# Kernel tuning notes

Hardware: AMD Instinct MI355X
Metric: run time of the kernel (lower is better)

Reference implementation:

```python
import jax, jax.numpy as jnp
import numpy as np

EMB = 1024
N_HEAD = 16
D_QK = 128  # emb_dim // h_qk
D_V = 128   # emb_dim // h_v


def setup_inputs() -> dict:
    key = jax.random.key(0)
    ks = jax.random.split(key, 9)
    s_in = 1.0 / np.sqrt(EMB)
    s_pr = 1.0 / np.sqrt(N_HEAD * D_V)
    return {
        "X": jax.random.normal(ks[0], (2, 2048, EMB), dtype=jnp.float32),
        "Wq": jax.random.uniform(ks[1], (EMB, N_HEAD * D_QK), jnp.float32, -s_in, s_in),
        "bq": jax.random.uniform(ks[2], (N_HEAD * D_QK,), jnp.float32, -s_in, s_in),
        "Wk": jax.random.uniform(ks[3], (EMB, N_HEAD * D_QK), jnp.float32, -s_in, s_in),
        "bk": jax.random.uniform(ks[4], (N_HEAD * D_QK,), jnp.float32, -s_in, s_in),
        "Wv": jax.random.uniform(ks[5], (EMB, N_HEAD * D_V), jnp.float32, -s_in, s_in),
        "bv": jax.random.uniform(ks[6], (N_HEAD * D_V,), jnp.float32, -s_in, s_in),
        "Wp": jax.random.uniform(ks[7], (N_HEAD * D_V, EMB), jnp.float32, -s_pr, s_pr),
        "bp": jax.random.uniform(ks[8], (EMB,), jnp.float32, -s_pr, s_pr),
    }


def reference(X, Wq, bq, Wk, bk, Wv, bv, Wp, bp):
    b, t, d = X.shape
    # projections -> (b, h, t, dh)
    Q = (X @ Wq + bq).reshape(b, t, N_HEAD, D_QK).transpose(0, 2, 1, 3)
    K = (X @ Wk + bk).reshape(b, t, N_HEAD, D_QK).transpose(0, 2, 1, 3)
    V = (X @ Wv + bv).reshape(b, t, N_HEAD, D_V).transpose(0, 2, 1, 3)
    scale = 1.0 / jnp.sqrt(jnp.asarray(D_QK, X.dtype))
    att = jnp.einsum("bhqd,bhkd->bhqk", Q, K) * scale  # (b,h,t,t)
    causal = jnp.tril(jnp.ones((t, t), dtype=bool))
    att = jnp.where(causal[None, None], att, jnp.asarray(-jnp.inf, att.dtype))
    att = jax.nn.softmax(att, axis=-1)
    y = jnp.einsum("bhqk,bhkd->bhqd", att, V)
    y = y.transpose(0, 2, 1, 3).reshape(b, t, N_HEAD * D_V)
    return y @ Wp + bp
```

## Files before the change

kernel.cpp:

```cpp
#include <hip/hip_runtime.h>
#include <hip/hip_bf16.h>
#include <math.h>

#define EMB   1024
#define NHEAD 16
#define DHEAD 128
#define TSEQ  2048
#define NB    2
#define MROWS (NB * TSEQ)
#define QKVN  (NHEAD * DHEAD)

typedef __bf16 bf16x8 __attribute__((ext_vector_type(8)));
typedef __bf16 bf16x4 __attribute__((ext_vector_type(4)));
typedef float  f32x4  __attribute__((ext_vector_type(4)));

__device__ __forceinline__ unsigned pk_bf16(float a, float b) {
  union { __bf16 h; unsigned short u; } ca, cb;
  ca.h = (__bf16)a; cb.h = (__bf16)b;
  return (unsigned)ca.u | ((unsigned)cb.u << 16);
}

__global__ __launch_bounds__(256) void prep(
    const float* __restrict__ X,
    const float* __restrict__ Wq, const float* __restrict__ Wk,
    const float* __restrict__ Wv, const float* __restrict__ Wp,
    __bf16* __restrict__ Xb, __bf16* __restrict__ Wqt, __bf16* __restrict__ Wkt,
    __bf16* __restrict__ Wvt, __bf16* __restrict__ Wpt) {
  const int z = blockIdx.z;
  if (z == 4) {
    size_t id = ((size_t)(blockIdx.y * 64 + blockIdx.x)) * 2048 + threadIdx.x * 8;
    float4 v0 = *(const float4*)(X + id);
    float4 v1 = *(const float4*)(X + id + 4);
    bf16x8 o = {(__bf16)v0.x, (__bf16)v0.y, (__bf16)v0.z, (__bf16)v0.w,
                (__bf16)v1.x, (__bf16)v1.y, (__bf16)v1.z, (__bf16)v1.w};
    *(bf16x8*)(Xb + id) = o;
    return;
  }
  __shared__ __bf16 tile[32][33];
  const float* in; __bf16* out; int K_, N_, k0, n0;
  if (z < 3) {
    in = z == 0 ? Wq : z == 1 ? Wk : Wv;
    out = z == 0 ? Wqt : z == 1 ? Wkt : Wvt;
    K_ = EMB; N_ = QKVN; k0 = blockIdx.y * 32; n0 = blockIdx.x * 32;
  } else {
    in = Wp; out = Wpt; K_ = QKVN; N_ = EMB; k0 = blockIdx.x * 32; n0 = blockIdx.y * 32;
  }
  const int c = threadIdx.x & 31, r = threadIdx.x >> 5;
#pragma unroll
  for (int i = 0; i < 4; ++i) {
    int kk = r + i * 8;
    tile[kk][c] = (__bf16)in[(size_t)(k0 + kk) * N_ + n0 + c];
  }
  __syncthreads();
#pragma unroll
  for (int i = 0; i < 4; ++i) {
    int nn = r + i * 8;
    out[(size_t)(n0 + nn) * K_ + k0 + c] = tile[c][nn];
  }
}

__device__ __forceinline__ void store1(float* p, float v) { *p = v; }
__device__ __forceinline__ void store1(__bf16* p, float v) { *p = (__bf16)v; }

template <int TM, typename OT, bool VT>
__device__ __forceinline__ void gemm_core(
    const __bf16* __restrict__ A, const __bf16* __restrict__ Bt,
    const float* __restrict__ bias, OT* __restrict__ C,
    int N, int K, int brow, int bcol, float osc,
    __bf16* As, __bf16* Bs) {
  const int tid = threadIdx.x;
  const int wv = tid >> 6, ln = tid & 63;
  const int cl = ln & 15, gp = ln >> 4;
  constexpr int SJ = (TM == 128) ? 4 : 2;
  const int rbase = (TM == 128) ? (wv >> 1) * 64 : 0;
  const int cbase = (TM == 128) ? (wv & 1) * 64 : wv * 32;

  f32x4 acc[4][SJ];
#pragma unroll
  for (int i = 0; i < 4; ++i)
#pragma unroll
    for (int j = 0; j < SJ; ++j) acc[i][j] = (f32x4){0.f, 0.f, 0.f, 0.f};

  for (int k0 = 0; k0 < K; k0 += 64) {
#pragma unroll
    for (int i = 0; i < TM / 32; ++i) {
      int idx = i * 256 + tid;
      int r = idx >> 3, cp = idx & 7, c = cp ^ (r & 7);
      __builtin_amdgcn_global_load_lds(
          (const __attribute__((address_space(1))) unsigned int*)(A + (size_t)(brow + r) * K + k0 + c * 8),
          (__attribute__((address_space(3))) unsigned int*)(As + (size_t)(i * 256 + wv * 64) * 8),
          16, 0, 0);
    }
#pragma unroll
    for (int i = 0; i < 4; ++i) {
      int idx = i * 256 + tid;
      int r = idx >> 3, cp = idx & 7, c = cp ^ (r & 7);
      __builtin_amdgcn_global_load_lds(
          (const __attribute__((address_space(1))) unsigned int*)(Bt + (size_t)(bcol + r) * K + k0 + c * 8),
          (__attribute__((address_space(3))) unsigned int*)(Bs + (size_t)(i * 256 + wv * 64) * 8),
          16, 0, 0);
    }
    __syncthreads();

#pragma unroll
    for (int kc = 0; kc < 2; ++kc) {
      bf16x8 af[4], bfr[SJ];
#pragma unroll
      for (int i = 0; i < 4; ++i) {
        int r = rbase + i * 16 + cl;
        int c = kc * 4 + gp;
        af[i] = *(const bf16x8*)(As + ((size_t)(r * 8 + (c ^ (r & 7)))) * 8);
      }
#pragma unroll
      for (int j = 0; j < SJ; ++j) {
        int r = cbase + j * 16 + cl;
        int c = kc * 4 + gp;
        bfr[j] = *(const bf16x8*)(Bs + ((size_t)(r * 8 + (c ^ (r & 7)))) * 8);
      }
#pragma unroll
      for (int i = 0; i < 4; ++i)
#pragma unroll
        for (int j = 0; j < SJ; ++j)
          acc[i][j] = __builtin_amdgcn_mfma_f32_16x16x32_bf16(af[i], bfr[j], acc[i][j], 0, 0, 0);
    }
    __syncthreads();
  }

  if constexpr (VT) {
#pragma unroll
    for (int j = 0; j < SJ; ++j) {
      int col = bcol + cbase + j * 16 + cl;
      float bb = bias[col];
      int hh = col >> 7, dh = col & 127;
#pragma unroll
      for (int i = 0; i < 4; ++i) {
        int row = brow + rbase + i * 16 + gp * 4;
        int bi = row >> 11, t = row & 2047;
        __bf16* p = (__bf16*)C + ((size_t)((bi * NHEAD + hh) * DHEAD + dh)) * TSEQ + t;
        bf16x4 st = {(__bf16)((acc[i][j][0] + bb) * osc), (__bf16)((acc[i][j][1] + bb) * osc),
                     (__bf16)((acc[i][j][2] + bb) * osc), (__bf16)((acc[i][j][3] + bb) * osc)};
        *(bf16x4*)p = st;
      }
    }
  } else {
#pragma unroll
    for (int j = 0; j < SJ; ++j) {
      int col = bcol + cbase + j * 16 + cl;
      float bb = bias[col];
#pragma unroll
      for (int i = 0; i < 4; ++i) {
#pragma unroll
        for (int rr = 0; rr < 4; ++rr) {
          int row = brow + rbase + i * 16 + gp * 4 + rr;
          store1(C + (size_t)row * N + col, (acc[i][j][rr] + bb) * osc);
        }
      }
    }
  }
}

__global__ __launch_bounds__(256) void gemm_qkv(
    const __bf16* __restrict__ A,
    const __bf16* __restrict__ Wqt, const __bf16* __restrict__ Wkt, const __bf16* __restrict__ Wvt,
    const float* __restrict__ bq, const float* __restrict__ bk, const float* __restrict__ bv,
    __bf16* __restrict__ Q, __bf16* __restrict__ Ko, __bf16* __restrict__ Vt) {
  __shared__ __bf16 As[8192], Bs[8192];
  const int z = blockIdx.z;
  if (z == 0) {
    gemm_core<128, __bf16, false>(A, Wqt, bq, Q, QKVN, EMB, blockIdx.y * 128, blockIdx.x * 128,
                                  0.08838834764831845f, As, Bs);
  } else if (z == 1) {
    gemm_core<128, __bf16, false>(A, Wkt, bk, Ko, QKVN, EMB, blockIdx.y * 128, blockIdx.x * 128,
                                  1.0f, As, Bs);
  } else {
    gemm_core<128, __bf16, true>(A, Wvt, bv, Vt, QKVN, EMB, blockIdx.y * 128, blockIdx.x * 128,
                                 1.0f, As, Bs);
  }
}

__global__ __launch_bounds__(256) void gemm_proj(
    const __bf16* __restrict__ A, const __bf16* __restrict__ Bt,
    const float* __restrict__ bias, float* __restrict__ C) {
  __shared__ __bf16 As[4096], Bs[8192];
  gemm_core<64, float, false>(A, Bt, bias, C, EMB, QKVN, blockIdx.y * 64, blockIdx.x * 128,
                              1.0f, As, Bs);
}

__device__ __forceinline__ void attn_stage(
    const __bf16* __restrict__ Kg, const __bf16* __restrict__ Vg,
    __bf16* Kbuf, __bf16* Vbuf, int kt, int wv, int ln) {
#pragma unroll
  for (int i = 0; i < 4; ++i) {
    int seg = wv * 4 + i;
    int u = seg * 4 + (ln >> 4);
    int slot = ln & 15;
    int xk = slot ^ (u & 15);
    __builtin_amdgcn_global_load_lds(
        (const __attribute__((address_space(1))) unsigned int*)(Kg + (size_t)(kt * 64 + u) * QKVN + xk * 8),
        (__attribute__((address_space(3))) unsigned int*)(Kbuf + seg * 512), 16, 0, 0);
    int d = 2 * u + (xk & 1), c2 = xk >> 1;
    __builtin_amdgcn_global_load_lds(
        (const __attribute__((address_space(1))) unsigned int*)(Vg + (size_t)d * TSEQ + kt * 64 + c2 * 8),
        (__attribute__((address_space(3))) unsigned int*)(Vbuf + seg * 512), 16, 0, 0);
  }
}

__global__ __launch_bounds__(256, 2) void attn_mfma(
    const __bf16* __restrict__ Qb, const __bf16* __restrict__ Kb,
    const __bf16* __restrict__ Vt, __bf16* __restrict__ Y) {
  __shared__ __bf16 Ks[2][8192];
  __shared__ __bf16 Vs[2][8192];

  const int tid = threadIdx.x;
  const int wv = tid >> 6, ln = tid & 63;
  const int cl = ln & 15, gp = ln >> 4;

  const int x = blockIdx.x;
  const int bh = x & 31;
  const int qt = 15 - (x >> 5);
  const int b = bh >> 4, h = bh & 15;
  const int ntiles = 2 * qt + 2;
  const int qloc = qt * 128 + wv * 32;
  const size_t grow = (size_t)b * TSEQ + qloc;

  bf16x8 qa[2][4];
#pragma unroll
  for (int i = 0; i < 2; ++i)
#pragma unroll
    for (int kc = 0; kc < 4; ++kc)
      qa[i][kc] = *(const bf16x8*)(Qb + (grow + i * 16 + cl) * QKVN + h * DHEAD + kc * 32 + gp * 8);

  f32x4 o[2][8];
#pragma unroll
  for (int i = 0; i < 2; ++i)
#pragma unroll
    for (int n = 0; n < 8; ++n) o[i][n] = (f32x4){0.f, 0.f, 0.f, 0.f};
  float l[2] = {0.f, 0.f};

  const __bf16* Kg = Kb + (size_t)b * TSEQ * QKVN + h * DHEAD;
  const __bf16* Vg = Vt + (size_t)bh * DHEAD * TSEQ;

  attn_stage(Kg, Vg, Ks[0], Vs[0], 0, wv, ln);
  __syncthreads();

  const int m0 = 32 * (gp & 1) + cl;
  const int m1 = m0 + 16;
  const bool hi = gp >= 2;

  for (int kt = 0; kt < ntiles; ++kt) {
    const int cur = kt & 1;
    if (kt + 1 < ntiles)
      attn_stage(Kg, Vg, Ks[cur ^ 1], Vs[cur ^ 1], kt + 1, wv, ln);

    if (kt * 64 <= qloc + 31) {
      f32x4 sacc[2][4];
#pragma unroll
      for (int i = 0; i < 2; ++i)
#pragma unroll
        for (int s = 0; s < 4; ++s) sacc[i][s] = (f32x4){0.f, 0.f, 0.f, 0.f};
#pragma unroll
      for (int kc = 0; kc < 4; ++kc) {
#pragma unroll
        for (int s = 0; s < 4; ++s) {
          int r = s * 16 + cl;
          bf16x8 kfr = *(const bf16x8*)(&Ks[cur][r * 128 + (((kc * 4 + gp) ^ (r & 15)) * 8)]);
          sacc[0][s] = __builtin_amdgcn_mfma_f32_16x16x32_bf16(kfr, qa[0][kc], sacc[0][s], 0, 0, 0);
          sacc[1][s] = __builtin_amdgcn_mfma_f32_16x16x32_bf16(kfr, qa[1][kc], sacc[1][s], 0, 0, 0);
        }
      }
      const bool diag = (kt * 64 + 63 > qloc);
      unsigned pk[2][4][2];
#pragma unroll
      for (int i = 0; i < 2; ++i) {
        float psum = 0.f;
        int q = qloc + i * 16 + cl;
#pragma unroll
        for (int s = 0; s < 4; ++s) {
          float e[4];
#pragma unroll
          for (int rg = 0; rg < 4; ++rg) {
            e[rg] = __expf(sacc[i][s][rg]);
            if (diag && (kt * 64 + s * 16 + gp * 4 + rg) > q) e[rg] = 0.f;
            psum += e[rg];
          }
          pk[i][s][0] = pk_bf16(e[0], e[1]);
          pk[i][s][1] = pk_bf16(e[2], e[3]);
        }
        psum += __shfl_xor(psum, 16, 64);
        psum += __shfl_xor(psum, 32, 64);
        l[i] += psum;
      }
#pragma unroll
      for (int k2 = 0; k2 < 2; ++k2) {
        union PU { unsigned u[4]; bf16x8 v; } pf[2];
#pragma unroll
        for (int i = 0; i < 2; ++i) {
          unsigned a0 = __shfl(pk[i][2 * k2][0], m0, 64);
          unsigned b0 = __shfl(pk[i][2 * k2 + 1][0], m0, 64);
          unsigned a1 = __shfl(pk[i][2 * k2][1], m0, 64);
          unsigned b1 = __shfl(pk[i][2 * k2 + 1][1], m0, 64);
          unsigned a2 = __shfl(pk[i][2 * k2][0], m1, 64);
          unsigned b2 = __shfl(pk[i][2 * k2 + 1][0], m1, 64);
          unsigned a3 = __shfl(pk[i][2 * k2][1], m1, 64);
          unsigned b3 = __shfl(pk[i][2 * k2 + 1][1], m1, 64);
          pf[i].u[0] = hi ? b0 : a0;
          pf[i].u[1] = hi ? b1 : a1;
          pf[i].u[2] = hi ? b2 : a2;
          pf[i].u[3] = hi ? b3 : a3;
        }
#pragma unroll
        for (int ds = 0; ds < 8; ++ds) {
          int d = ds * 16 + cl;
          int u = d >> 1;
          int xv = ((k2 * 4 + gp) << 1) | (d & 1);
          bf16x8 vfr = *(const bf16x8*)(&Vs[cur][u * 128 + ((xv ^ (u & 15)) * 8)]);
          o[0][ds] = __builtin_amdgcn_mfma_f32_16x16x32_bf16(vfr, pf[0].v, o[0][ds], 0, 0, 0);
          o[1][ds] = __builtin_amdgcn_mfma_f32_16x16x32_bf16(vfr, pf[1].v, o[1][ds], 0, 0, 0);
        }
      }
    }
    __syncthreads();
  }

#pragma unroll
  for (int i = 0; i < 2; ++i) {
    float inv = 1.0f / l[i];
    __bf16* yrow = Y + (grow + i * 16 + cl) * QKVN + h * DHEAD;
#pragma unroll
    for (int ds = 0; ds < 8; ++ds) {
      bf16x4 st = {(__bf16)(o[i][ds][0] * inv), (__bf16)(o[i][ds][1] * inv),
                   (__bf16)(o[i][ds][2] * inv), (__bf16)(o[i][ds][3] * inv)};
      *(bf16x4*)(yrow + ds * 16 + gp * 4) = st;
    }
  }
}

extern "C" void kernel_launch(void* const* d_in, const int* in_sizes, int n_in,
                              void* d_out, int out_size, void* d_ws, size_t ws_size,
                              hipStream_t stream) {
  const float* X  = (const float*)d_in[0];
  const float* Wq = (const float*)d_in[1];
  const float* bq = (const float*)d_in[2];
  const float* Wk = (const float*)d_in[3];
  const float* bk = (const float*)d_in[4];
  const float* Wv = (const float*)d_in[5];
  const float* bv = (const float*)d_in[6];
  const float* Wp = (const float*)d_in[7];
  const float* bp = (const float*)d_in[8];
  float* out = (float*)d_out;

  const size_t xsz = (size_t)MROWS * EMB;
  const size_t wsz = (size_t)EMB * QKVN;
  const size_t msz = (size_t)MROWS * QKVN;
  __bf16* Xb  = (__bf16*)d_ws;
  __bf16* Wqt = Xb + xsz;
  __bf16* Wkt = Wqt + wsz;
  __bf16* Wvt = Wkt + wsz;
  __bf16* Wpt = Wvt + wsz;
  __bf16* Qb  = Wpt + wsz;
  __bf16* Kb  = Qb + msz;
  __bf16* Vtb = Kb + msz;
  __bf16* Yb  = Vtb + msz;

  dim3 blk(256);

  prep<<<dim3(64, 32, 5), blk, 0, stream>>>(X, Wq, Wk, Wv, Wp, Xb, Wqt, Wkt, Wvt, Wpt);

  gemm_qkv<<<dim3(QKVN / 128, MROWS / 128, 3), blk, 0, stream>>>(
      Xb, Wqt, Wkt, Wvt, bq, bk, bv, Qb, Kb, Vtb);

  attn_mfma<<<dim3(512), blk, 0, stream>>>(Qb, Kb, Vtb, Yb);

  gemm_proj<<<dim3(EMB / 128, MROWS / 64), blk, 0, stream>>>(Yb, Wpt, bp, out);
}
```

Before: 284.9 us.

## Halve attention block to 64 query rows with single-buffered V staging

The attention kernel now runs 2-wave blocks covering 64 query rows, launched as 1024 blocks instead of 512 4-wave blocks of 128 rows. The per-wave skip of fully masked tiles is dropped. V shared memory drops to one buffer, reloaded after an extra barrier once the PV MFMAs finish, while K stays double-buffered. The goal is finer causal load balance and lower LDS use for more resident blocks. The cost is that the V load is no longer overlapped with compute, each iteration has an extra barrier, and K/V tiles are fetched by twice as many blocks.

```diff
diff --git a/kernel.cpp b/kernel.cpp
--- a/kernel.cpp
+++ b/kernel.cpp
@@ -186,18 +186,28 @@
                               1.0f, As, Bs);
 }
 
-__device__ __forceinline__ void attn_stage(
-    const __bf16* __restrict__ Kg, const __bf16* __restrict__ Vg,
-    __bf16* Kbuf, __bf16* Vbuf, int kt, int wv, int ln) {
-#pragma unroll
-  for (int i = 0; i < 4; ++i) {
-    int seg = wv * 4 + i;
+__device__ __forceinline__ void stage_K(
+    const __bf16* __restrict__ Kg, __bf16* Kbuf, int kt, int wv, int ln) {
+#pragma unroll
+  for (int i = 0; i < 8; ++i) {
+    int seg = wv * 8 + i;
     int u = seg * 4 + (ln >> 4);
     int slot = ln & 15;
     int xk = slot ^ (u & 15);
     __builtin_amdgcn_global_load_lds(
         (const __attribute__((address_space(1))) unsigned int*)(Kg + (size_t)(kt * 64 + u) * QKVN + xk * 8),
         (__attribute__((address_space(3))) unsigned int*)(Kbuf + seg * 512), 16, 0, 0);
+  }
+}
+
+__device__ __forceinline__ void stage_V(
+    const __bf16* __restrict__ Vg, __bf16* Vbuf, int kt, int wv, int ln) {
+#pragma unroll
+  for (int i = 0; i < 8; ++i) {
+    int seg = wv * 8 + i;
+    int u = seg * 4 + (ln >> 4);
+    int slot = ln & 15;
+    int xk = slot ^ (u & 15);
     int d = 2 * u + (xk & 1), c2 = xk >> 1;
     __builtin_amdgcn_global_load_lds(
         (const __attribute__((address_space(1))) unsigned int*)(Vg + (size_t)d * TSEQ + kt * 64 + c2 * 8),
@@ -205,11 +215,11 @@
   }
 }
 
-__global__ __launch_bounds__(256, 2) void attn_mfma(
+__global__ __launch_bounds__(128) void attn_mfma(
     const __bf16* __restrict__ Qb, const __bf16* __restrict__ Kb,
     const __bf16* __restrict__ Vt, __bf16* __restrict__ Y) {
   __shared__ __bf16 Ks[2][8192];
-  __shared__ __bf16 Vs[2][8192];
+  __shared__ __bf16 Vs[8192];
 
   const int tid = threadIdx.x;
   const int wv = tid >> 6, ln = tid & 63;
@@ -217,10 +227,10 @@
 
   const int x = blockIdx.x;
   const int bh = x & 31;
-  const int qt = 15 - (x >> 5);
+  const int qt = 31 - (x >> 5);
   const int b = bh >> 4, h = bh & 15;
-  const int ntiles = 2 * qt + 2;
-  const int qloc = qt * 128 + wv * 32;
+  const int ntiles = qt + 1;
+  const int qloc = qt * 64 + wv * 32;
   const size_t grow = (size_t)b * TSEQ + qloc;
 
   bf16x8 qa[2][4];
@@ -240,7 +250,8 @@
   const __bf16* Kg = Kb + (size_t)b * TSEQ * QKVN + h * DHEAD;
   const __bf16* Vg = Vt + (size_t)bh * DHEAD * TSEQ;
 
-  attn_stage(Kg, Vg, Ks[0], Vs[0], 0, wv, ln);
+  stage_K(Kg, Ks[0], 0, wv, ln);
+  stage_V(Vg, Vs, 0, wv, ln);
   __syncthreads();
 
   const int m0 = 32 * (gp & 1) + cl;
@@ -250,75 +261,76 @@
   for (int kt = 0; kt < ntiles; ++kt) {
     const int cur = kt & 1;
     if (kt + 1 < ntiles)
-      attn_stage(Kg, Vg, Ks[cur ^ 1], Vs[cur ^ 1], kt + 1, wv, ln);
-
-    if (kt * 64 <= qloc + 31) {
-      f32x4 sacc[2][4];
-#pragma unroll
-      for (int i = 0; i < 2; ++i)
-#pragma unroll
-        for (int s = 0; s < 4; ++s) sacc[i][s] = (f32x4){0.f, 0.f, 0.f, 0.f};
-#pragma unroll
-      for (int kc = 0; kc < 4; ++kc) {
-#pragma unroll
-        for (int s = 0; s < 4; ++s) {
-          int r = s * 16 + cl;
-          bf16x8 kfr = *(const bf16x8*)(&Ks[cur][r * 128 + (((kc * 4 + gp) ^ (r & 15)) * 8)]);
-          sacc[0][s] = __builtin_amdgcn_mfma_f32_16x16x32_bf16(kfr, qa[0][kc], sacc[0][s], 0, 0, 0);
-          sacc[1][s] = __builtin_amdgcn_mfma_f32_16x16x32_bf16(kfr, qa[1][kc], sacc[1][s], 0, 0, 0);
+      stage_K(Kg, Ks[cur ^ 1], kt + 1, wv, ln);
+
+    f32x4 sacc[2][4];
+#pragma unroll
+    for (int i = 0; i < 2; ++i)
+#pragma unroll
+      for (int s = 0; s < 4; ++s) sacc[i][s] = (f32x4){0.f, 0.f, 0.f, 0.f};
+#pragma unroll
+    for (int kc = 0; kc < 4; ++kc) {
+#pragma unroll
+      for (int s = 0; s < 4; ++s) {
+        int r = s * 16 + cl;
+        bf16x8 kfr = *(const bf16x8*)(&Ks[cur][r * 128 + (((kc * 4 + gp) ^ (r & 15)) * 8)]);
+        sacc[0][s] = __builtin_amdgcn_mfma_f32_16x16x32_bf16(kfr, qa[0][kc], sacc[0][s], 0, 0, 0);
+        sacc[1][s] = __builtin_amdgcn_mfma_f32_16x16x32_bf16(kfr, qa[1][kc], sacc[1][s], 0, 0, 0);
+      }
+    }
+    const bool diag = (kt * 64 + 63 > qloc);
+    unsigned pk[2][4][2];
+#pragma unroll
+    for (int i = 0; i < 2; ++i) {
+      float psum = 0.f;
+      int q = qloc + i * 16 + cl;
+#pragma unroll
+      for (int s = 0; s < 4; ++s) {
+        float e[4];
+#pragma unroll
+        for (int rg = 0; rg < 4; ++rg) {
+          e[rg] = __expf(sacc[i][s][rg]);
+          if (diag && (kt * 64 + s * 16 + gp * 4 + rg) > q) e[rg] = 0.f;
+          psum += e[rg];
         }
-      }
-      const bool diag = (kt * 64 + 63 > qloc);
-      unsigned pk[2][4][2];
+        pk[i][s][0] = pk_bf16(e[0], e[1]);
+        pk[i][s][1] = pk_bf16(e[2], e[3]);
+      }
+      psum += __shfl_xor(psum, 16, 64);
+      psum += __shfl_xor(psum, 32, 64);
+      l[i] += psum;
+    }
+#pragma unroll
+    for (int k2 = 0; k2 < 2; ++k2) {
+      union PU { unsigned u[4]; bf16x8 v; } pf[2];
 #pragma unroll
       for (int i = 0; i < 2; ++i) {
-        float psum = 0.f;
-        int q = qloc + i * 16 + cl;
-#pragma unroll
-        for (int s = 0; s < 4; ++s) {
-          float e[4];
-#pragma unroll
-          for (int rg = 0; rg < 4; ++rg) {
-            e[rg] = __expf(sacc[i][s][rg]);
-            if (diag && (kt * 64 + s * 16 + gp * 4 + rg) > q) e[rg] = 0.f;
-            psum += e[rg];
-          }
-          pk[i][s][0] = pk_bf16(e[0], e[1]);
-          pk[i][s][1] = pk_bf16(e[2], e[3]);
-        }
-        psum += __shfl_xor(psum, 16, 64);
-        psum += __shfl_xor(psum, 32, 64);
-        l[i] += psum;
-      }
-#pragma unroll
-      for (int k2 = 0; k2 < 2; ++k2) {
-        union PU { unsigned u[4]; bf16x8 v; } pf[2];
-#pragma unroll
-        for (int i = 0; i < 2; ++i) {
-          unsigned a0 = __shfl(pk[i][2 * k2][0], m0, 64);
-          unsigned b0 = __shfl(pk[i][2 * k2 + 1][0], m0, 64);
-          unsigned a1 = __shfl(pk[i][2 * k2][1], m0, 64);
-          unsigned b1 = __shfl(pk[i][2 * k2 + 1][1], m0, 64);
-          unsigned a2 = __shfl(pk[i][2 * k2][0], m1, 64);
-          unsigned b2 = __shfl(pk[i][2 * k2 + 1][0], m1, 64);
-          unsigned a3 = __shfl(pk[i][2 * k2][1], m1, 64);
-          unsigned b3 = __shfl(pk[i][2 * k2 + 1][1], m1, 64);
-          pf[i].u[0] = hi ? b0 : a0;
-          pf[i].u[1] = hi ? b1 : a1;
-          pf[i].u[2] = hi ? b2 : a2;
-          pf[i].u[3] = hi ? b3 : a3;
-        }
-#pragma unroll
-        for (int ds = 0; ds < 8; ++ds) {
-          int d = ds * 16 + cl;
-          int u = d >> 1;
-          int xv = ((k2 * 4 + gp) << 1) | (d & 1);
-          bf16x8 vfr = *(const bf16x8*)(&Vs[cur][u * 128 + ((xv ^ (u & 15)) * 8)]);
-          o[0][ds] = __builtin_amdgcn_mfma_f32_16x16x32_bf16(vfr, pf[0].v, o[0][ds], 0, 0, 0);
-          o[1][ds] = __builtin_amdgcn_mfma_f32_16x16x32_bf16(vfr, pf[1].v, o[1][ds], 0, 0, 0);
-        }
-      }
-    }
+        unsigned a0 = __shfl(pk[i][2 * k2][0], m0, 64);
+        unsigned b0 = __shfl(pk[i][2 * k2 + 1][0], m0, 64);
+        unsigned a1 = __shfl(pk[i][2 * k2][1], m0, 64);
+        unsigned b1 = __shfl(pk[i][2 * k2 + 1][1], m0, 64);
+        unsigned a2 = __shfl(pk[i][2 * k2][0], m1, 64);
+        unsigned b2 = __shfl(pk[i][2 * k2 + 1][0], m1, 64);
+        unsigned a3 = __shfl(pk[i][2 * k2][1], m1, 64);
+        unsigned b3 = __shfl(pk[i][2 * k2 + 1][1], m1, 64);
+        pf[i].u[0] = hi ? b0 : a0;
+        pf[i].u[1] = hi ? b1 : a1;
+        pf[i].u[2] = hi ? b2 : a2;
+        pf[i].u[3] = hi ? b3 : a3;
+      }
+#pragma unroll
+      for (int ds = 0; ds < 8; ++ds) {
+        int d = ds * 16 + cl;
+        int u = d >> 1;
+        int xv = ((k2 * 4 + gp) << 1) | (d & 1);
+        bf16x8 vfr = *(const bf16x8*)(&Vs[u * 128 + ((xv ^ (u & 15)) * 8)]);
+        o[0][ds] = __builtin_amdgcn_mfma_f32_16x16x32_bf16(vfr, pf[0].v, o[0][ds], 0, 0, 0);
+        o[1][ds] = __builtin_amdgcn_mfma_f32_16x16x32_bf16(vfr, pf[1].v, o[1][ds], 0, 0, 0);
+      }
+    }
+    __syncthreads();
+    if (kt + 1 < ntiles)
+      stage_V(Vg, Vs, kt + 1, wv, ln);
     __syncthreads();
   }
 
@@ -369,7 +381,7 @@
   gemm_qkv<<<dim3(QKVN / 128, MROWS / 128, 3), blk, 0, stream>>>(
       Xb, Wqt, Wkt, Wvt, bq, bk, bv, Qb, Kb, Vtb);
 
-  attn_mfma<<<dim3(512), blk, 0, stream>>>(Qb, Kb, Vtb, Yb);
+  attn_mfma<<<dim3(1024), dim3(128), 0, stream>>>(Qb, Kb, Vtb, Yb);
 
   gemm_proj<<<dim3(EMB / 128, MROWS / 64), blk, 0, stream>>>(Yb, Wpt, bp, out);
 }
```

New measurement: 294.7 us. 3.4% more time.

## Store Q/K/V in MFMA fragment-blocked layout and use single-wave attention blocks

Applied to the files above, without the earlier changes.

The QKV GEMM epilogue now writes Q, K and V directly in a pre-swizzled, fragment-ordered blocked layout, so every lane loads its MFMA operand with a contiguous 16-byte read. The attention kernel drops the LDS staging, double buffering and block-wide syncs. It uses 64-thread blocks (one wave per 32 queries, 2048 blocks) that read K/V fragments straight from global memory and cache. This trades LDS reuse across the four waves for finer-grained scheduling and no barriers, but K/V are now re-read by every wave. The epilogue's scattered scalar bf16 stores could also cost more in the GEMM.

```diff
diff --git a/kernel.cpp b/kernel.cpp
--- a/kernel.cpp
+++ b/kernel.cpp
@@ -59,10 +59,7 @@
   }
 }
 
-__device__ __forceinline__ void store1(float* p, float v) { *p = v; }
-__device__ __forceinline__ void store1(__bf16* p, float v) { *p = (__bf16)v; }
-
-template <int TM, typename OT, bool VT>
+template <int TM, int MODE, typename OT>
 __device__ __forceinline__ void gemm_core(
     const __bf16* __restrict__ A, const __bf16* __restrict__ Bt,
     const float* __restrict__ bias, OT* __restrict__ C,
@@ -126,33 +123,35 @@
     __syncthreads();
   }
 
-  if constexpr (VT) {
-#pragma unroll
-    for (int j = 0; j < SJ; ++j) {
-      int col = bcol + cbase + j * 16 + cl;
-      float bb = bias[col];
-      int hh = col >> 7, dh = col & 127;
-#pragma unroll
-      for (int i = 0; i < 4; ++i) {
-        int row = brow + rbase + i * 16 + gp * 4;
-        int bi = row >> 11, t = row & 2047;
-        __bf16* p = (__bf16*)C + ((size_t)((bi * NHEAD + hh) * DHEAD + dh)) * TSEQ + t;
-        bf16x4 st = {(__bf16)((acc[i][j][0] + bb) * osc), (__bf16)((acc[i][j][1] + bb) * osc),
-                     (__bf16)((acc[i][j][2] + bb) * osc), (__bf16)((acc[i][j][3] + bb) * osc)};
-        *(bf16x4*)p = st;
-      }
-    }
-  } else {
-#pragma unroll
-    for (int j = 0; j < SJ; ++j) {
-      int col = bcol + cbase + j * 16 + cl;
-      float bb = bias[col];
-#pragma unroll
-      for (int i = 0; i < 4; ++i) {
-#pragma unroll
-        for (int rr = 0; rr < 4; ++rr) {
-          int row = brow + rbase + i * 16 + gp * 4 + rr;
-          store1(C + (size_t)row * N + col, (acc[i][j][rr] + bb) * osc);
+#pragma unroll
+  for (int j = 0; j < SJ; ++j) {
+    int col = bcol + cbase + j * 16 + cl;
+    float bb = bias[col];
+    int h = col >> 7, d = col & 127;
+#pragma unroll
+    for (int i = 0; i < 4; ++i) {
+      int row0 = brow + rbase + i * 16 + gp * 4;
+#pragma unroll
+      for (int rr = 0; rr < 4; ++rr) {
+        float val = (acc[i][j][rr] + bb) * osc;
+        if constexpr (MODE == 3) {
+          C[(size_t)(row0 + rr) * N + col] = val;
+        } else {
+          int row = row0 + rr;
+          int b = row >> 11, tok = row & 2047;
+          int bh = b * NHEAD + h;
+          size_t idx;
+          if constexpr (MODE == 0) {
+            idx = (((size_t)bh * 64 + (tok >> 5)) * 8 + ((tok >> 4) & 1) * 4 + (d >> 5)) * 512
+                + (((d >> 3) & 3) * 16 + (tok & 15)) * 8 + (d & 7);
+          } else if constexpr (MODE == 1) {
+            idx = (((size_t)bh * 32 + (tok >> 6)) * 16 + ((tok >> 4) & 3) * 4 + (d >> 5)) * 512
+                + (((d >> 3) & 3) * 16 + (tok & 15)) * 8 + (d & 7);
+          } else {
+            idx = (((size_t)bh * 32 + (tok >> 6)) * 16 + (d >> 4) * 2 + ((tok >> 5) & 1)) * 512
+                + (((tok >> 3) & 3) * 16 + (d & 15)) * 8 + (tok & 7);
+          }
+          ((__bf16*)C)[idx] = (__bf16)val;
         }
       }
     }
@@ -163,18 +162,18 @@
     const __bf16* __restrict__ A,
     const __bf16* __restrict__ Wqt, const __bf16* __restrict__ Wkt, const __bf16* __restrict__ Wvt,
     const float* __restrict__ bq, const float* __restrict__ bk, const float* __restrict__ bv,
-    __bf16* __restrict__ Q, __bf16* __restrict__ Ko, __bf16* __restrict__ Vt) {
+    __bf16* __restrict__ Qblk, __bf16* __restrict__ Kblk, __bf16* __restrict__ Vblk) {
   __shared__ __bf16 As[8192], Bs[8192];
   const int z = blockIdx.z;
   if (z == 0) {
-    gemm_core<128, __bf16, false>(A, Wqt, bq, Q, QKVN, EMB, blockIdx.y * 128, blockIdx.x * 128,
-                                  0.08838834764831845f, As, Bs);
+    gemm_core<128, 0, __bf16>(A, Wqt, bq, Qblk, QKVN, EMB, blockIdx.y * 128, blockIdx.x * 128,
+                              0.08838834764831845f, As, Bs);
   } else if (z == 1) {
-    gemm_core<128, __bf16, false>(A, Wkt, bk, Ko, QKVN, EMB, blockIdx.y * 128, blockIdx.x * 128,
-                                  1.0f, As, Bs);
+    gemm_core<128, 1, __bf16>(A, Wkt, bk, Kblk, QKVN, EMB, blockIdx.y * 128, blockIdx.x * 128,
+                              1.0f, As, Bs);
   } else {
-    gemm_core<128, __bf16, true>(A, Wvt, bv, Vt, QKVN, EMB, blockIdx.y * 128, blockIdx.x * 128,
-                                 1.0f, As, Bs);
+    gemm_core<128, 2, __bf16>(A, Wvt, bv, Vblk, QKVN, EMB, blockIdx.y * 128, blockIdx.x * 128,
+                              1.0f, As, Bs);
   }
 }
 
@@ -182,53 +181,31 @@
     const __bf16* __restrict__ A, const __bf16* __restrict__ Bt,
     const float* __restrict__ bias, float* __restrict__ C) {
   __shared__ __bf16 As[4096], Bs[8192];
-  gemm_core<64, float, false>(A, Bt, bias, C, EMB, QKVN, blockIdx.y * 64, blockIdx.x * 128,
-                              1.0f, As, Bs);
-}
-
-__device__ __forceinline__ void attn_stage(
-    const __bf16* __restrict__ Kg, const __bf16* __restrict__ Vg,
-    __bf16* Kbuf, __bf16* Vbuf, int kt, int wv, int ln) {
-#pragma unroll
-  for (int i = 0; i < 4; ++i) {
-    int seg = wv * 4 + i;
-    int u = seg * 4 + (ln >> 4);
-    int slot = ln & 15;
-    int xk = slot ^ (u & 15);
-    __builtin_amdgcn_global_load_lds(
-        (const __attribute__((address_space(1))) unsigned int*)(Kg + (size_t)(kt * 64 + u) * QKVN + xk * 8),
-        (__attribute__((address_space(3))) unsigned int*)(Kbuf + seg * 512), 16, 0, 0);
-    int d = 2 * u + (xk & 1), c2 = xk >> 1;
-    __builtin_amdgcn_global_load_lds(
-        (const __attribute__((address_space(1))) unsigned int*)(Vg + (size_t)d * TSEQ + kt * 64 + c2 * 8),
-        (__attribute__((address_space(3))) unsigned int*)(Vbuf + seg * 512), 16, 0, 0);
-  }
-}
-
-__global__ __launch_bounds__(256, 2) void attn_mfma(
-    const __bf16* __restrict__ Qb, const __bf16* __restrict__ Kb,
-    const __bf16* __restrict__ Vt, __bf16* __restrict__ Y) {
-  __shared__ __bf16 Ks[2][8192];
-  __shared__ __bf16 Vs[2][8192];
-
-  const int tid = threadIdx.x;
-  const int wv = tid >> 6, ln = tid & 63;
+  gemm_core<64, 3, float>(A, Bt, bias, C, EMB, QKVN, blockIdx.y * 64, blockIdx.x * 128,
+                          1.0f, As, Bs);
+}
+
+__global__ __launch_bounds__(64) void attn_mfma(
+    const __bf16* __restrict__ Qblk, const __bf16* __restrict__ Kblk,
+    const __bf16* __restrict__ Vblk, __bf16* __restrict__ Y) {
+  const int ln = threadIdx.x;
   const int cl = ln & 15, gp = ln >> 4;
 
   const int x = blockIdx.x;
   const int bh = x & 31;
-  const int qt = 15 - (x >> 5);
+  const int qt = 63 - (x >> 5);
   const int b = bh >> 4, h = bh & 15;
-  const int ntiles = 2 * qt + 2;
-  const int qloc = qt * 128 + wv * 32;
+  const int ntiles = (qt >> 1) + 1;
+  const int qloc = qt * 32;
   const size_t grow = (size_t)b * TSEQ + qloc;
 
   bf16x8 qa[2][4];
+  const __bf16* qb = Qblk + (((size_t)bh * 64 + qt) * 8) * 512 + ln * 8;
 #pragma unroll
   for (int i = 0; i < 2; ++i)
 #pragma unroll
     for (int kc = 0; kc < 4; ++kc)
-      qa[i][kc] = *(const bf16x8*)(Qb + (grow + i * 16 + cl) * QKVN + h * DHEAD + kc * 32 + gp * 8);
+      qa[i][kc] = *(const bf16x8*)(qb + (i * 4 + kc) * 512);
 
   f32x4 o[2][8];
 #pragma unroll
@@ -236,90 +213,82 @@
 #pragma unroll
     for (int n = 0; n < 8; ++n) o[i][n] = (f32x4){0.f, 0.f, 0.f, 0.f};
   float l[2] = {0.f, 0.f};
-
-  const __bf16* Kg = Kb + (size_t)b * TSEQ * QKVN + h * DHEAD;
-  const __bf16* Vg = Vt + (size_t)bh * DHEAD * TSEQ;
-
-  attn_stage(Kg, Vg, Ks[0], Vs[0], 0, wv, ln);
-  __syncthreads();
 
   const int m0 = 32 * (gp & 1) + cl;
   const int m1 = m0 + 16;
   const bool hi = gp >= 2;
 
   for (int kt = 0; kt < ntiles; ++kt) {
-    const int cur = kt & 1;
-    if (kt + 1 < ntiles)
-      attn_stage(Kg, Vg, Ks[cur ^ 1], Vs[cur ^ 1], kt + 1, wv, ln);
-
-    if (kt * 64 <= qloc + 31) {
-      f32x4 sacc[2][4];
-#pragma unroll
-      for (int i = 0; i < 2; ++i)
-#pragma unroll
-        for (int s = 0; s < 4; ++s) sacc[i][s] = (f32x4){0.f, 0.f, 0.f, 0.f};
+    const __bf16* kb = Kblk + (((size_t)bh * 32 + kt) * 16) * 512 + ln * 8;
+    const __bf16* vb = Vblk + (((size_t)bh * 32 + kt) * 16) * 512 + ln * 8;
+
+    f32x4 sacc[2][4];
+#pragma unroll
+    for (int i = 0; i < 2; ++i)
+#pragma unroll
+      for (int s = 0; s < 4; ++s) sacc[i][s] = (f32x4){0.f, 0.f, 0.f, 0.f};
+#pragma unroll
+    for (int s = 0; s < 4; ++s) {
+      bf16x8 kfr[4];
+#pragma unroll
+      for (int kc = 0; kc < 4; ++kc)
+        kfr[kc] = *(const bf16x8*)(kb + (s * 4 + kc) * 512);
 #pragma unroll
       for (int kc = 0; kc < 4; ++kc) {
-#pragma unroll
-        for (int s = 0; s < 4; ++s) {
-          int r = s * 16 + cl;
-          bf16x8 kfr = *(const bf16x8*)(&Ks[cur][r * 128 + (((kc * 4 + gp) ^ (r & 15)) * 8)]);
-          sacc[0][s] = __builtin_amdgcn_mfma_f32_16x16x32_bf16(kfr, qa[0][kc], sacc[0][s], 0, 0, 0);
-          sacc[1][s] = __builtin_amdgcn_mfma_f32_16x16x32_bf16(kfr, qa[1][kc], sacc[1][s], 0, 0, 0);
+        sacc[0][s] = __builtin_amdgcn_mfma_f32_16x16x32_bf16(kfr[kc], qa[0][kc], sacc[0][s], 0, 0, 0);
+        sacc[1][s] = __builtin_amdgcn_mfma_f32_16x16x32_bf16(kfr[kc], qa[1][kc], sacc[1][s], 0, 0, 0);
+      }
+    }
+    const bool diag = (kt * 64 + 63 > qloc);
+    unsigned pk[2][4][2];
+#pragma unroll
+    for (int i = 0; i < 2; ++i) {
+      float psum = 0.f;
+      int q = qloc + i * 16 + cl;
+#pragma unroll
+      for (int s = 0; s < 4; ++s) {
+        float e[4];
+#pragma unroll
+        for (int rg = 0; rg < 4; ++rg) {
+          e[rg] = __expf(sacc[i][s][rg]);
+          if (diag && (kt * 64 + s * 16 + gp * 4 + rg) > q) e[rg] = 0.f;
+          psum += e[rg];
         }
-      }
-      const bool diag = (kt * 64 + 63 > qloc);
-      unsigned pk[2][4][2];
+        pk[i][s][0] = pk_bf16(e[0], e[1]);
+        pk[i][s][1] = pk_bf16(e[2], e[3]);
+      }
+      psum += __shfl_xor(psum, 16, 64);
+      psum += __shfl_xor(psum, 32, 64);
+      l[i] += psum;
+    }
+#pragma unroll
+    for (int k2 = 0; k2 < 2; ++k2) {
+      bf16x8 vfr[8];
+#pragma unroll
+      for (int ds = 0; ds < 8; ++ds)
+        vfr[ds] = *(const bf16x8*)(vb + (ds * 2 + k2) * 512);
+      union PU { unsigned u[4]; bf16x8 v; } pf[2];
 #pragma unroll
       for (int i = 0; i < 2; ++i) {
-        float psum = 0.f;
-        int q = qloc + i * 16 + cl;
-#pragma unroll
-        for (int s = 0; s < 4; ++s) {
-          float e[4];
-#pragma unroll
-          for (int rg = 0; rg < 4; ++rg) {
-            e[rg] = __expf(sacc[i][s][rg]);
-            if (diag && (kt * 64 + s * 16 + gp * 4 + rg) > q) e[rg] = 0.f;
-            psum += e[rg];
-          }
-          pk[i][s][0] = pk_bf16(e[0], e[1]);
-          pk[i][s][1] = pk_bf16(e[2], e[3]);
-        }
-        psum += __shfl_xor(psum, 16, 64);
-        psum += __shfl_xor(psum, 32, 64);
-        l[i] += psum;
-      }
-#pragma unroll
-      for (int k2 = 0; k2 < 2; ++k2) {
-        union PU { unsigned u[4]; bf16x8 v; } pf[2];
-#pragma unroll
-        for (int i = 0; i < 2; ++i) {
-          unsigned a0 = __shfl(pk[i][2 * k2][0], m0, 64);
-          unsigned b0 = __shfl(pk[i][2 * k2 + 1][0], m0, 64);
-          unsigned a1 = __shfl(pk[i][2 * k2][1], m0, 64);
-          unsigned b1 = __shfl(pk[i][2 * k2 + 1][1], m0, 64);
-          unsigned a2 = __shfl(pk[i][2 * k2][0], m1, 64);
-          unsigned b2 = __shfl(pk[i][2 * k2 + 1][0], m1, 64);
-          unsigned a3 = __shfl(pk[i][2 * k2][1], m1, 64);
-          unsigned b3 = __shfl(pk[i][2 * k2 + 1][1], m1, 64);
-          pf[i].u[0] = hi ? b0 : a0;
-          pf[i].u[1] = hi ? b1 : a1;
-          pf[i].u[2] = hi ? b2 : a2;
-          pf[i].u[3] = hi ? b3 : a3;
-        }
-#pragma unroll
-        for (int ds = 0; ds < 8; ++ds) {
-          int d = ds * 16 + cl;
-          int u = d >> 1;
-          int xv = ((k2 * 4 + gp) << 1) | (d & 1);
-          bf16x8 vfr = *(const bf16x8*)(&Vs[cur][u * 128 + ((xv ^ (u & 15)) * 8)]);
-          o[0][ds] = __builtin_amdgcn_mfma_f32_16x16x32_bf16(vfr, pf[0].v, o[0][ds], 0, 0, 0);
-          o[1][ds] = __builtin_amdgcn_mfma_f32_16x16x32_bf16(vfr, pf[1].v, o[1][ds], 0, 0, 0);
-        }
-      }
-    }
-    __syncthreads();
+        unsigned a0 = __shfl(pk[i][2 * k2][0], m0, 64);
+        unsigned b0 = __shfl(pk[i][2 * k2 + 1][0], m0, 64);
+        unsigned a1 = __shfl(pk[i][2 * k2][1], m0, 64);
+        unsigned b1 = __shfl(pk[i][2 * k2 + 1][1], m0, 64);
+        unsigned a2 = __shfl(pk[i][2 * k2][0], m1, 64);
+        unsigned b2 = __shfl(pk[i][2 * k2 + 1][0], m1, 64);
+        unsigned a3 = __shfl(pk[i][2 * k2][1], m1, 64);
+        unsigned b3 = __shfl(pk[i][2 * k2 + 1][1], m1, 64);
+        pf[i].u[0] = hi ? b0 : a0;
+        pf[i].u[1] = hi ? b1 : a1;
+        pf[i].u[2] = hi ? b2 : a2;
+        pf[i].u[3] = hi ? b3 : a3;
+      }
+#pragma unroll
+      for (int ds = 0; ds < 8; ++ds) {
+        o[0][ds] = __builtin_amdgcn_mfma_f32_16x16x32_bf16(vfr[ds], pf[0].v, o[0][ds], 0, 0, 0);
+        o[1][ds] = __builtin_amdgcn_mfma_f32_16x16x32_bf16(vfr[ds], pf[1].v, o[1][ds], 0, 0, 0);
+      }
+    }
   }
 
 #pragma unroll
@@ -352,24 +321,24 @@
   const size_t xsz = (size_t)MROWS * EMB;
   const size_t wsz = (size_t)EMB * QKVN;
   const size_t msz = (size_t)MROWS * QKVN;
-  __bf16* Xb  = (__bf16*)d_ws;
-  __bf16* Wqt = Xb + xsz;
-  __bf16* Wkt = Wqt + wsz;
-  __bf16* Wvt = Wkt + wsz;
-  __bf16* Wpt = Wvt + wsz;
-  __bf16* Qb  = Wpt + wsz;
-  __bf16* Kb  = Qb + msz;
-  __bf16* Vtb = Kb + msz;
-  __bf16* Yb  = Vtb + msz;
+  __bf16* Xb   = (__bf16*)d_ws;
+  __bf16* Wqt  = Xb + xsz;
+  __bf16* Wkt  = Wqt + wsz;
+  __bf16* Wvt  = Wkt + wsz;
+  __bf16* Wpt  = Wvt + wsz;
+  __bf16* Qblk = Wpt + wsz;
+  __bf16* Kblk = Qblk + msz;
+  __bf16* Vblk = Kblk + msz;
+  __bf16* Yb   = Vblk + msz;
 
   dim3 blk(256);
 
   prep<<<dim3(64, 32, 5), blk, 0, stream>>>(X, Wq, Wk, Wv, Wp, Xb, Wqt, Wkt, Wvt, Wpt);
 
   gemm_qkv<<<dim3(QKVN / 128, MROWS / 128, 3), blk, 0, stream>>>(
-      Xb, Wqt, Wkt, Wvt, bq, bk, bv, Qb, Kb, Vtb);
-
-  attn_mfma<<<dim3(512), blk, 0, stream>>>(Qb, Kb, Vtb, Yb);
+      Xb, Wqt, Wkt, Wvt, bq, bk, bv, Qblk, Kblk, Vblk);
+
+  attn_mfma<<<dim3(2048), dim3(64), 0, stream>>>(Qblk, Kblk, Vblk, Yb);
 
   gemm_proj<<<dim3(EMB / 128, MROWS / 64), blk, 0, stream>>>(Yb, Wpt, bp, out);
 }
```

Result: slower. 303.4 us (+6.5%).
